# Kernel tuning notes

Hardware: AMD Instinct MI355X
Metric: run time of the kernel (lower is better)

Reference implementation:

```python
import jax, jax.numpy as jnp
import numpy as np

N_NODES = 100000
N_EDGES = 800000
IN_CH, HID_CH, OUT_CH = 128, 256, 128


def setup_inputs() -> dict:
    key = jax.random.key(0)
    ks = jax.random.split(key, 8)
    x = jax.random.normal(ks[0], (N_NODES, IN_CH), dtype=jnp.float32)
    edge_index = jax.random.randint(ks[1], (2, N_EDGES), 0, N_NODES, dtype=jnp.int64)
    def lin(k, fan_in, fan_out):
        bound = 1.0 / np.sqrt(fan_in)
        return jax.random.uniform(k, (fan_out, fan_in), minval=-bound, maxval=bound, dtype=jnp.float32)
    # PyG SAGEConv: lin_l (neighbor branch, with bias), lin_r (root branch, no bias)
    W1l = lin(ks[2], IN_CH, HID_CH)
    b1l = jnp.zeros((HID_CH,), dtype=jnp.float32)
    W1r = lin(ks[3], IN_CH, HID_CH)
    W2l = lin(ks[4], HID_CH, OUT_CH)
    b2l = jnp.zeros((OUT_CH,), dtype=jnp.float32)
    W2r = lin(ks[5], HID_CH, OUT_CH)
    return {"x": x, "edge_index": edge_index, "W1l": W1l, "b1l": b1l, "W1r": W1r,
            "W2l": W2l, "b2l": b2l, "W2r": W2r}


def _sage_conv(x, src, dst, Wl, bl, Wr):
    # mean-aggregate messages x[src] at dst, then lin_l(agg) + lin_r(x)
    msgs = x[src]                                        # [E, C]
    summed = jax.ops.segment_sum(msgs, dst, num_segments=N_NODES)
    cnt = jax.ops.segment_sum(jnp.ones((src.shape[0],), dtype=x.dtype), dst, num_segments=N_NODES)
    mean = summed / jnp.maximum(cnt, 1.0)[:, None]       # [N, C]
    return mean @ Wl.T + bl + x @ Wr.T


def reference(x, edge_index, W1l, b1l, W1r, W2l, b2l, W2r):
    src, dst = edge_index[0], edge_index[1]
    h = _sage_conv(x, src, dst, W1l, b1l, W1r)
    h = jax.nn.relu(h)
    # dropout is identity in eval mode (F.dropout with training=False)
    out = _sage_conv(h, src, dst, W2l, b2l, W2r)
    return out
```

## Files before the change

kernel.cpp:

```cpp
#include <hip/hip_runtime.h>

#define N_NODES 100000
#define N_EDGES 800000
#define SCAN_CHUNK 1024
#define SCAN_NB ((N_NODES + SCAN_CHUNK - 1) / SCAN_CHUNK)
#define ROWS_PER_BLK 391
#define TILES 25

typedef __attribute__((ext_vector_type(8))) _Float16 f16x8;
typedef __attribute__((ext_vector_type(4))) _Float16 f16x4;
typedef __attribute__((ext_vector_type(4))) float f32x4;

__global__ void count_int_k(const int* __restrict__ dst, int* __restrict__ cnt, int E) {
    int i = blockIdx.x * blockDim.x + threadIdx.x;
    if (i < E) atomicAdd(&cnt[dst[i]], 1);
}

__global__ __launch_bounds__(256) void scan1_k(const int* __restrict__ cnt,
                                               int* __restrict__ offs,
                                               int* __restrict__ bsums, int N) {
    __shared__ int s[256];
    int t = threadIdx.x;
    int base = blockIdx.x * SCAN_CHUNK + t * 4;
    int v0 = (base + 0 < N) ? cnt[base + 0] : 0;
    int v1 = (base + 1 < N) ? cnt[base + 1] : 0;
    int v2 = (base + 2 < N) ? cnt[base + 2] : 0;
    int v3 = (base + 3 < N) ? cnt[base + 3] : 0;
    int tsum = v0 + v1 + v2 + v3;
    s[t] = tsum;
    __syncthreads();
    for (int off = 1; off < 256; off <<= 1) {
        int val = (t >= off) ? s[t - off] : 0;
        __syncthreads();
        s[t] += val;
        __syncthreads();
    }
    int excl = s[t] - tsum;
    if (base + 0 < N) offs[base + 0] = excl;
    if (base + 1 < N) offs[base + 1] = excl + v0;
    if (base + 2 < N) offs[base + 2] = excl + v0 + v1;
    if (base + 3 < N) offs[base + 3] = excl + v0 + v1 + v2;
    if (t == 255) bsums[blockIdx.x] = s[255];
}

__global__ __launch_bounds__(256) void scan2_k(const int* __restrict__ bsums,
                                               int* __restrict__ boffs, int nb) {
    __shared__ int s[256];
    int t = threadIdx.x;
    int v = (t < nb) ? bsums[t] : 0;
    s[t] = v;
    __syncthreads();
    for (int off = 1; off < 256; off <<= 1) {
        int val = (t >= off) ? s[t - off] : 0;
        __syncthreads();
        s[t] += val;
        __syncthreads();
    }
    if (t < nb) boffs[t] = s[t] - v;
}

__global__ void scan3_k(int* __restrict__ offs, int* __restrict__ cursor,
                        const int* __restrict__ boffs, int N, int E) {
    int i = blockIdx.x * blockDim.x + threadIdx.x;
    if (i < N) {
        int v = offs[i] + boffs[i >> 10];
        offs[i] = v;
        cursor[i] = v;
    }
    if (i == 0) offs[N] = E;
}

__global__ void fill_k(const int* __restrict__ src, const int* __restrict__ dst,
                       int* __restrict__ cursor, int* __restrict__ perm, int E) {
    int e = blockIdx.x * blockDim.x + threadIdx.x;
    if (e < E) {
        int d = dst[e];
        int slot = atomicAdd(&cursor[d], 1);
        perm[slot] = src[e];
    }
}

__global__ __launch_bounds__(256) void cvt_f16_k(const float* __restrict__ in,
                                                 _Float16* __restrict__ outp, int n8) {
    int i = blockIdx.x * blockDim.x + threadIdx.x;
    if (i >= n8) return;
    const float4* p = (const float4*)in + (long long)i * 2;
    float4 v0 = p[0], v1 = p[1];
    f16x8 h;
    h[0] = (_Float16)v0.x; h[1] = (_Float16)v0.y;
    h[2] = (_Float16)v0.z; h[3] = (_Float16)v0.w;
    h[4] = (_Float16)v1.x; h[5] = (_Float16)v1.y;
    h[6] = (_Float16)v1.z; h[7] = (_Float16)v1.w;
    *(f16x8*)&outp[(long long)i * 8] = h;
}

__global__ __launch_bounds__(256) void cvt_w4_k(const float* __restrict__ w0,
                                                const float* __restrict__ w1,
                                                const float* __restrict__ w2,
                                                const float* __restrict__ w3,
                                                _Float16* __restrict__ o0,
                                                _Float16* __restrict__ o1,
                                                _Float16* __restrict__ o2,
                                                _Float16* __restrict__ o3) {
    int i = blockIdx.x * blockDim.x + threadIdx.x;
    int wsel = i >> 12;
    int j = i & 4095;
    const float* in; _Float16* outp;
    if (wsel == 0)      { in = w0; outp = o0; }
    else if (wsel == 1) { in = w1; outp = o1; }
    else if (wsel == 2) { in = w2; outp = o2; }
    else                { in = w3; outp = o3; }
    const float4* p = (const float4*)in + (long long)j * 2;
    float4 v0 = p[0], v1 = p[1];
    f16x8 h;
    h[0] = (_Float16)v0.x; h[1] = (_Float16)v0.y;
    h[2] = (_Float16)v0.z; h[3] = (_Float16)v0.w;
    h[4] = (_Float16)v1.x; h[5] = (_Float16)v1.y;
    h[6] = (_Float16)v1.z; h[7] = (_Float16)v1.w;
    *(f16x8*)&outp[(long long)j * 8] = h;
}

__global__ __launch_bounds__(256) void aggmean_k(const _Float16* __restrict__ feat16,
                                                 const int* __restrict__ perm,
                                                 const int* __restrict__ offs,
                                                 _Float16* __restrict__ m16, int N) {
    int tid = threadIdx.x;
    int node = blockIdx.x * 16 + (tid >> 4);
    int q = tid & 15;
    if (node >= N) return;
    int beg = offs[node], end = offs[node + 1];
    float a[8], b[8];
#pragma unroll
    for (int k = 0; k < 8; k++) { a[k] = 0.0f; b[k] = 0.0f; }
    int i = beg;
    for (; i + 1 < end; i += 2) {
        f16x8 v0 = *(const f16x8*)&feat16[(long long)perm[i] * 128 + q * 8];
        f16x8 v1 = *(const f16x8*)&feat16[(long long)perm[i + 1] * 128 + q * 8];
#pragma unroll
        for (int k = 0; k < 8; k++) { a[k] += (float)v0[k]; b[k] += (float)v1[k]; }
    }
    if (i < end) {
        f16x8 v0 = *(const f16x8*)&feat16[(long long)perm[i] * 128 + q * 8];
#pragma unroll
        for (int k = 0; k < 8; k++) a[k] += (float)v0[k];
    }
    float rc = 1.0f / fmaxf((float)(end - beg), 1.0f);
    f16x8 v;
#pragma unroll
    for (int k = 0; k < 8; k++) v[k] = (_Float16)((a[k] + b[k]) * rc);
    *(f16x8*)&m16[(long long)node * 128 + q * 8] = v;
}

__global__ __launch_bounds__(256) void aggout_k(const _Float16* __restrict__ g16,
                                                const int* __restrict__ perm,
                                                const int* __restrict__ offs,
                                                const _Float16* __restrict__ r2h,
                                                const float* __restrict__ b2l,
                                                float* __restrict__ out, int N) {
    int tid = threadIdx.x;
    int node = blockIdx.x * 16 + (tid >> 4);
    int q = tid & 15;
    if (node >= N) return;
    int beg = offs[node], end = offs[node + 1];
    float a[8], b[8];
#pragma unroll
    for (int k = 0; k < 8; k++) { a[k] = 0.0f; b[k] = 0.0f; }
    int i = beg;
    for (; i + 1 < end; i += 2) {
        f16x8 v0 = *(const f16x8*)&g16[(long long)perm[i] * 128 + q * 8];
        f16x8 v1 = *(const f16x8*)&g16[(long long)perm[i + 1] * 128 + q * 8];
#pragma unroll
        for (int k = 0; k < 8; k++) { a[k] += (float)v0[k]; b[k] += (float)v1[k]; }
    }
    if (i < end) {
        f16x8 v0 = *(const f16x8*)&g16[(long long)perm[i] * 128 + q * 8];
#pragma unroll
        for (int k = 0; k < 8; k++) a[k] += (float)v0[k];
    }
    float rc = 1.0f / fmaxf((float)(end - beg), 1.0f);
    f16x8 rv = *(const f16x8*)&r2h[(long long)node * 128 + q * 8];
    float4 bv0 = ((const float4*)b2l)[q * 2];
    float4 bv1 = ((const float4*)b2l)[q * 2 + 1];
    float4 o0, o1;
    o0.x = (a[0] + b[0]) * rc + (float)rv[0] + bv0.x;
    o0.y = (a[1] + b[1]) * rc + (float)rv[1] + bv0.y;
    o0.z = (a[2] + b[2]) * rc + (float)rv[2] + bv0.z;
    o0.w = (a[3] + b[3]) * rc + (float)rv[3] + bv0.w;
    o1.x = (a[4] + b[4]) * rc + (float)rv[4] + bv1.x;
    o1.y = (a[5] + b[5]) * rc + (float)rv[5] + bv1.y;
    o1.z = (a[6] + b[6]) * rc + (float)rv[6] + bv1.z;
    o1.w = (a[7] + b[7]) * rc + (float)rv[7] + bv1.w;
    ((float4*)out)[(long long)node * 32 + q * 2]     = o0;
    ((float4*)out)[(long long)node * 32 + q * 2 + 1] = o1;
}

__device__ inline void gload16(const void* g, void* l) {
    __builtin_amdgcn_global_load_lds(
        (const __attribute__((address_space(1))) unsigned int*)g,
        (__attribute__((address_space(3))) unsigned int*)l,
        16, 0, 0);
}

template <int LAYER>
__global__ __launch_bounds__(512, 1) void gemm_stream_k(
        const _Float16* __restrict__ Ap0, const _Float16* __restrict__ Ap1,
        const _Float16* __restrict__ Bp0, const _Float16* __restrict__ Bp1,
        const float* __restrict__ bias,
        _Float16* __restrict__ O1h,
        _Float16* __restrict__ OH, int N) {
    __shared__ _Float16 Bs[256 * 256];
    __shared__ _Float16 As3[3][16 * 256];

    const int mbase = blockIdx.x * ROWS_PER_BLK;
    const int rend = min(mbase + ROWS_PER_BLK, N);
    const int tid = threadIdx.x;
    const int lane = tid & 63;
    const int wid = tid >> 6;
    const int lr = lane & 15, lg = lane >> 4;
    const int r2 = lane >> 5;
    const int scs = lane & 31;

    auto STAGE_A = [&](int tt, int bi) {
        int lrow = wid * 2 + r2;
        int ck = scs ^ (lrow & 15);
        int gn = mbase + tt * 16 + lrow;
        if (gn < N) {
            const _Float16* src;
            if constexpr (LAYER == 1)
                src = (ck < 16) ? (Ap0 + (long long)gn * 128 + ck * 8)
                                : (Ap1 + (long long)gn * 128 + (ck - 16) * 8);
            else
                src = Ap0 + (long long)gn * 256 + ck * 8;
            gload16(src, &As3[bi][wid * 512]);
        }
    };

#pragma unroll
    for (int it = 0; it < 16; ++it) {
        int seg = wid * 16 + it;
        int col = seg * 2 + r2;
        int ck = scs ^ (col & 15);
        const _Float16* src;
        if constexpr (LAYER == 1)
            src = (ck < 16) ? (Bp0 + (long long)col * 128 + ck * 8)
                            : (Bp1 + (long long)col * 128 + (ck - 16) * 8);
        else
            src = (col < 128) ? (Bp0 + (long long)col * 256 + ck * 8)
                              : (Bp1 + (long long)(col - 128) * 256 + ck * 8);
        gload16(src, &Bs[seg * 512]);
    }
    STAGE_A(0, 0);
    STAGE_A(1, 1);
    asm volatile("s_waitcnt vmcnt(1)" ::: "memory");
    __builtin_amdgcn_s_barrier();

#pragma unroll 1
    for (int t = 0; t < TILES; ++t) {
        if (t + 2 < TILES) {
            STAGE_A(t + 2, (t + 2) % 3);
            asm volatile("s_waitcnt vmcnt(2)" ::: "memory");
        } else if (t + 1 < TILES) {
            asm volatile("s_waitcnt vmcnt(1)" ::: "memory");
        } else {
            asm volatile("s_waitcnt vmcnt(0)" ::: "memory");
        }
        __builtin_amdgcn_sched_barrier(0);
        __builtin_amdgcn_s_barrier();

        const _Float16* Ab = &As3[t % 3][0];
        f32x4 acc[2];
        acc[0] = (f32x4)0.0f;
        acc[1] = (f32x4)0.0f;
#pragma unroll
        for (int ks = 0; ks < 8; ++ks) {
            int c = ks * 4 + lg;
            f16x8 af = *(const f16x8*)&Ab[lr * 256 + (c ^ lr) * 8];
#pragma unroll
            for (int fc = 0; fc < 2; ++fc) {
                int col = wid * 32 + fc * 16 + lr;
                f16x8 bf = *(const f16x8*)&Bs[col * 256 + (c ^ (col & 15)) * 8];
                acc[fc] = __builtin_amdgcn_mfma_f32_16x16x32_f16(af, bf, acc[fc], 0, 0, 0);
            }
        }

#pragma unroll
        for (int fc = 0; fc < 2; ++fc) {
            int col = wid * 32 + fc * 16 + lr;
            if constexpr (LAYER == 1) {
                float bv = bias[col];
#pragma unroll
                for (int j = 0; j < 4; ++j) {
                    int row = mbase + t * 16 + lg * 4 + j;
                    if (row < rend)
                        OH[(long long)row * 256 + col] =
                            (_Float16)fmaxf(acc[fc][j] + bv, 0.0f);
                }
            } else {
                _Float16* dp = (col < 128) ? OH : O1h;
                int dcol = col & 127;
#pragma unroll
                for (int j = 0; j < 4; ++j) {
                    int row = mbase + t * 16 + lg * 4 + j;
                    if (row < rend)
                        dp[(long long)row * 128 + dcol] = (_Float16)acc[fc][j];
                }
            }
        }
        __builtin_amdgcn_s_barrier();
    }
}

extern "C" void kernel_launch(void* const* d_in, const int* in_sizes, int n_in,
                              void* d_out, int out_size, void* d_ws, size_t ws_size,
                              hipStream_t stream) {
    const float* x   = (const float*)d_in[0];
    const int*   ei  = (const int*)d_in[1];
    const float* W1l = (const float*)d_in[2];
    const float* b1l = (const float*)d_in[3];
    const float* W1r = (const float*)d_in[4];
    const float* W2l = (const float*)d_in[5];
    const float* b2l = (const float*)d_in[6];
    const float* W2r = (const float*)d_in[7];
    float* out = (float*)d_out;

    const int N = N_NODES, E = N_EDGES;
    const int* srcI = ei;
    const int* dstI = ei + E;

    char* ws = (char*)d_ws;
    size_t off = 0;
    auto alloc = [&](size_t bytes) {
        size_t o = off;
        off += (bytes + 511) & ~(size_t)511;
        return o;
    };
    size_t off_cnt   = alloc((size_t)N * 4);
    size_t off_offs  = alloc((size_t)(N + 1) * 4);
    size_t off_cur   = alloc((size_t)N * 4);
    size_t off_bsum  = alloc((size_t)SCAN_NB * 4);
    size_t off_boff  = alloc((size_t)SCAN_NB * 4);
    size_t off_perm  = alloc((size_t)E * 4);
    size_t off_x16   = alloc((size_t)N * 128 * 2);
    size_t off_m16   = alloc((size_t)N * 128 * 2);
    size_t off_h16   = alloc((size_t)N * 256 * 2);
    size_t off_g16   = alloc((size_t)N * 128 * 2);
    size_t off_r2    = alloc((size_t)N * 128 * 2);
    size_t off_w     = alloc((size_t)4 * 32768 * 2);
    int*      cntI = (int*)(ws + off_cnt);
    int*      offs = (int*)(ws + off_offs);
    int*      cur  = (int*)(ws + off_cur);
    int*      bsum = (int*)(ws + off_bsum);
    int*      boff = (int*)(ws + off_boff);
    int*      perm = (int*)(ws + off_perm);
    _Float16* x16  = (_Float16*)(ws + off_x16);
    _Float16* m16  = (_Float16*)(ws + off_m16);
    _Float16* h16  = (_Float16*)(ws + off_h16);
    _Float16* g16  = (_Float16*)(ws + off_g16);
    _Float16* r2h  = (_Float16*)(ws + off_r2);
    _Float16* wbuf = (_Float16*)(ws + off_w);
    const int WSZ = 32768;
    _Float16* w1l16 = wbuf;            _Float16* w1r16 = wbuf + WSZ;
    _Float16* w2l16 = wbuf + 2 * WSZ;  _Float16* w2r16 = wbuf + 3 * WSZ;

    (void)hipMemsetAsync(cntI, 0, (size_t)N * 4, stream);
    count_int_k<<<(E + 255) / 256, 256, 0, stream>>>(dstI, cntI, E);
    scan1_k<<<SCAN_NB, 256, 0, stream>>>(cntI, offs, bsum, N);
    scan2_k<<<1, 256, 0, stream>>>(bsum, boff, SCAN_NB);
    scan3_k<<<(N + 255) / 256, 256, 0, stream>>>(offs, cur, boff, N, E);
    fill_k<<<(E + 255) / 256, 256, 0, stream>>>(srcI, dstI, cur, perm, E);

    {
        int n8x = N * 16;
        cvt_f16_k<<<(n8x + 255) / 256, 256, 0, stream>>>(x, x16, n8x);
        cvt_w4_k<<<16384 / 256, 256, 0, stream>>>(W1l, W1r, W2l, W2r,
                                                  w1l16, w1r16, w2l16, w2r16);
    }

    aggmean_k<<<(N + 15) / 16, 256, 0, stream>>>(x16, perm, offs, m16, N);
    gemm_stream_k<1><<<256, 512, 0, stream>>>(m16, x16, w1l16, w1r16,
                                              b1l, nullptr, h16, N);

    gemm_stream_k<2><<<256, 512, 0, stream>>>(h16, h16, w2l16, w2r16,
                                              nullptr, r2h, g16, N);
    aggout_k<<<(N + 15) / 16, 256, 0, stream>>>(g16, perm, offs, r2h, b2l, out, N);
}
```

Measured before the change: 261.0 us.

## Split GEMM blocks across output column halves and shrink LDS for two blocks per CU

Each GEMM block now computes only half of the 256 output columns, so the grid doubles to 512 blocks and the B tile held in LDS halves. The A tile ring drops from triple to double buffering, and launch bounds now ask for two blocks per CU. The aim is more blocks in flight per CU to hide latency and better use of the 256 CUs. The cost is that each A row tile is loaded twice, once per column half, and prefetch depth within a block is shallower.

```diff
diff --git a/kernel.cpp b/kernel.cpp
--- a/kernel.cpp
+++ b/kernel.cpp
@@ -202,16 +202,18 @@
 }
 
 template <int LAYER>
-__global__ __launch_bounds__(512, 1) void gemm_stream_k(
+__global__ __launch_bounds__(512, 2) void gemm_stream_k(
         const _Float16* __restrict__ Ap0, const _Float16* __restrict__ Ap1,
         const _Float16* __restrict__ Bp0, const _Float16* __restrict__ Bp1,
         const float* __restrict__ bias,
         _Float16* __restrict__ O1h,
         _Float16* __restrict__ OH, int N) {
-    __shared__ _Float16 Bs[256 * 256];
-    __shared__ _Float16 As3[3][16 * 256];
-
-    const int mbase = blockIdx.x * ROWS_PER_BLK;
+    __shared__ _Float16 Bs[128 * 256];
+    __shared__ _Float16 As2[2][16 * 256];
+
+    const int rb = blockIdx.x >> 1;
+    const int cb = blockIdx.x & 1;
+    const int mbase = rb * ROWS_PER_BLK;
     const int rend = min(mbase + ROWS_PER_BLK, N);
     const int tid = threadIdx.x;
     const int lane = tid & 63;
@@ -231,35 +233,32 @@
                                 : (Ap1 + (long long)gn * 128 + (ck - 16) * 8);
             else
                 src = Ap0 + (long long)gn * 256 + ck * 8;
-            gload16(src, &As3[bi][wid * 512]);
+            gload16(src, &As2[bi][wid * 512]);
         }
     };
 
 #pragma unroll
-    for (int it = 0; it < 16; ++it) {
-        int seg = wid * 16 + it;
-        int col = seg * 2 + r2;
-        int ck = scs ^ (col & 15);
+    for (int it = 0; it < 8; ++it) {
+        int seg = wid * 8 + it;
+        int lcol = seg * 2 + r2;
+        int col = cb * 128 + lcol;
+        int ck = scs ^ (lcol & 15);
         const _Float16* src;
         if constexpr (LAYER == 1)
             src = (ck < 16) ? (Bp0 + (long long)col * 128 + ck * 8)
                             : (Bp1 + (long long)col * 128 + (ck - 16) * 8);
         else
-            src = (col < 128) ? (Bp0 + (long long)col * 256 + ck * 8)
-                              : (Bp1 + (long long)(col - 128) * 256 + ck * 8);
+            src = ((cb == 0) ? Bp0 : Bp1) + (long long)lcol * 256 + ck * 8;
         gload16(src, &Bs[seg * 512]);
     }
     STAGE_A(0, 0);
-    STAGE_A(1, 1);
-    asm volatile("s_waitcnt vmcnt(1)" ::: "memory");
+    asm volatile("s_waitcnt vmcnt(0)" ::: "memory");
     __builtin_amdgcn_s_barrier();
 
 #pragma unroll 1
     for (int t = 0; t < TILES; ++t) {
-        if (t + 2 < TILES) {
-            STAGE_A(t + 2, (t + 2) % 3);
-            asm volatile("s_waitcnt vmcnt(2)" ::: "memory");
-        } else if (t + 1 < TILES) {
+        if (t + 1 < TILES) {
+            STAGE_A(t + 1, (t + 1) & 1);
             asm volatile("s_waitcnt vmcnt(1)" ::: "memory");
         } else {
             asm volatile("s_waitcnt vmcnt(0)" ::: "memory");
@@ -267,25 +266,19 @@
         __builtin_amdgcn_sched_barrier(0);
         __builtin_amdgcn_s_barrier();
 
-        const _Float16* Ab = &As3[t % 3][0];
-        f32x4 acc[2];
-        acc[0] = (f32x4)0.0f;
-        acc[1] = (f32x4)0.0f;
+        const _Float16* Ab = &As2[t & 1][0];
+        f32x4 acc = (f32x4)0.0f;
 #pragma unroll
         for (int ks = 0; ks < 8; ++ks) {
             int c = ks * 4 + lg;
             f16x8 af = *(const f16x8*)&Ab[lr * 256 + (c ^ lr) * 8];
-#pragma unroll
-            for (int fc = 0; fc < 2; ++fc) {
-                int col = wid * 32 + fc * 16 + lr;
-                f16x8 bf = *(const f16x8*)&Bs[col * 256 + (c ^ (col & 15)) * 8];
-                acc[fc] = __builtin_amdgcn_mfma_f32_16x16x32_f16(af, bf, acc[fc], 0, 0, 0);
-            }
+            int lcol = wid * 16 + lr;
+            f16x8 bf = *(const f16x8*)&Bs[lcol * 256 + (c ^ (lcol & 15)) * 8];
+            acc = __builtin_amdgcn_mfma_f32_16x16x32_f16(af, bf, acc, 0, 0, 0);
         }
 
-#pragma unroll
-        for (int fc = 0; fc < 2; ++fc) {
-            int col = wid * 32 + fc * 16 + lr;
+        {
+            int col = cb * 128 + wid * 16 + lr;
             if constexpr (LAYER == 1) {
                 float bv = bias[col];
 #pragma unroll
@@ -293,16 +286,16 @@
                     int row = mbase + t * 16 + lg * 4 + j;
                     if (row < rend)
                         OH[(long long)row * 256 + col] =
-                            (_Float16)fmaxf(acc[fc][j] + bv, 0.0f);
+                            (_Float16)fmaxf(acc[j] + bv, 0.0f);
                 }
             } else {
-                _Float16* dp = (col < 128) ? OH : O1h;
-                int dcol = col & 127;
+                _Float16* dp = (cb == 0) ? OH : O1h;
+                int dcol = wid * 16 + lr;
 #pragma unroll
                 for (int j = 0; j < 4; ++j) {
                     int row = mbase + t * 16 + lg * 4 + j;
                     if (row < rend)
-                        dp[(long long)row * 128 + dcol] = (_Float16)acc[fc][j];
+                        dp[(long long)row * 128 + dcol] = (_Float16)acc[j];
                 }
             }
         }
@@ -377,10 +370,10 @@
     }
 
     aggmean_k<<<(N + 15) / 16, 256, 0, stream>>>(x16, perm, offs, m16, N);
-    gemm_stream_k<1><<<256, 512, 0, stream>>>(m16, x16, w1l16, w1r16,
+    gemm_stream_k<1><<<512, 512, 0, stream>>>(m16, x16, w1l16, w1r16,
                                               b1l, nullptr, h16, N);
 
-    gemm_stream_k<2><<<256, 512, 0, stream>>>(h16, h16, w2l16, w2r16,
+    gemm_stream_k<2><<<512, 512, 0, stream>>>(h16, h16, w2l16, w2r16,
                                               nullptr, r2h, g16, N);
     aggout_k<<<(N + 15) / 16, 256, 0, stream>>>(g16, perm, offs, r2h, b2l, out, N);
 }
```

After: 259.4 us. No clear change (-0.6%).
